# Optimization experiments

Hardware: AMD Instinct MI355X
Metric: run time of the kernel (lower is better)

Reference implementation:

```python
import jax, jax.numpy as jnp
import numpy as np
from jax import lax

E = 8          # num_experts
K = 2          # top-k
TASKS = 8
GATE_DIM = 16
# (in, expand, out, kernel, stride) per MoE stage
STAGES = [(3, 32, 16, 7, 2), (16, 64, 32, 3, 1), (32, 128, 64, 3, 2), (64, 256, 64, 3, 1), (64, 128, 32, 3, 1)]
DN = ('NCHW', 'OIHW', 'NCHW')


def _pw(x, w):
    return lax.conv_general_dilated(x, w, (1, 1), 'VALID', dimension_numbers=DN)


def _dw(x, w, s):
    p = w.shape[-1] // 2
    return lax.conv_general_dilated(x, w, (s, s), [(p, p), (p, p)], dimension_numbers=DN, feature_group_count=x.shape[1])


def _gn(x, scale, bias):
    # GroupNorm with num_groups = C // 4, eps = 1e-5 (torch default)
    B, C, H, W = x.shape
    G = C // 4
    xr = x.reshape(B, G, -1)
    m = xr.mean(-1, keepdims=True)
    v = xr.var(-1, keepdims=True)
    xn = ((xr - m) * lax.rsqrt(v + 1e-5)).reshape(B, C, H, W)
    return xn * scale[None, :, None, None] + bias[None, :, None, None]


def _dsc(x, p, stride):
    # DSCBlock: pw-conv -> GN -> SiLU -> dw-conv -> GN -> SiLU -> pw-conv -> GN
    w1, s1, b1, w2, s2, b2, w3, s3, b3 = p
    x = jax.nn.silu(_gn(_pw(x, w1), s1, b1))
    x = jax.nn.silu(_gn(_dw(x, w2, stride), s2, b2))
    return _gn(_pw(x, w3), s3, b3)


def _moe(gate_input, x, wg, p, stride, task_bh):
    # task-conditioned top-k softmax gating (noisy_gating=False, all aux loss weights 0)
    logits = gate_input @ wg[task_bh]                      # (B, E)
    probs = jax.nn.softmax(logits, axis=-1)
    topv, topi = lax.top_k(probs, K)
    topv = topv / topv.sum(-1, keepdims=True)              # renormalize top-k gates
    Bn = gate_input.shape[0]
    dense = jnp.zeros_like(probs).at[jnp.arange(Bn)[:, None], topi].set(topv)
    eo = jax.vmap(lambda pe: _dsc(x, pe, stride))(p)       # (E, B, C, H, W)
    return jnp.einsum('be,ebchw->bchw', dense, eo)


def _forward(fl, task_bh):
    gi, xi, ppe = fl[0], fl[1], fl[2]
    x = xi
    for i, (_, _, _, _, s) in enumerate(STAGES):
        base = 3 + i * 10
        wg = fl[base]
        p = tuple(fl[base + 1: base + 10])
        x = _moe(gi, x, wg, p, s, task_bh)
    Bn = x.shape[0]
    # patchify: (B,32,20,20) -> unfold(2,4,4).unfold(3,4,4) -> permute -> (B,25,512)
    patches = x.reshape(Bn, 32, 5, 4, 5, 4).transpose(0, 1, 2, 4, 3, 5)  # (B,32,5,5,4,4)
    patches = patches.transpose(0, 2, 3, 4, 5, 1).reshape(Bn, 25, 512)
    return patches + ppe


def setup_inputs():
    key = jax.random.key(0)
    ks = iter(jax.random.split(key, 256))
    B = 64
    d = {}
    d['gate_input'] = jax.random.normal(next(ks), (B, GATE_DIM), jnp.float32)
    d['expert_input'] = jax.random.normal(next(ks), (B, 3, 80, 80), jnp.float32)
    d['patch_pos_embed'] = 0.02 * jax.random.normal(next(ks), (1, 25, 512), jnp.float32)
    for i, (cin, exp, cout, k, s) in enumerate(STAGES, 1):
        d[f's{i}_wg'] = 0.1 * jax.random.normal(next(ks), (TASKS, GATE_DIM, E), jnp.float32)
        d[f's{i}_w1'] = jax.random.normal(next(ks), (E, exp, cin, 1, 1), jnp.float32) / np.sqrt(cin)
        d[f's{i}_g1s'] = 1.0 + 0.1 * jax.random.normal(next(ks), (E, exp), jnp.float32)
        d[f's{i}_g1b'] = 0.1 * jax.random.normal(next(ks), (E, exp), jnp.float32)
        d[f's{i}_w2'] = jax.random.normal(next(ks), (E, exp, 1, k, k), jnp.float32) / k
        d[f's{i}_g2s'] = 1.0 + 0.1 * jax.random.normal(next(ks), (E, exp), jnp.float32)
        d[f's{i}_g2b'] = 0.1 * jax.random.normal(next(ks), (E, exp), jnp.float32)
        d[f's{i}_w3'] = jax.random.normal(next(ks), (E, cout, exp, 1, 1), jnp.float32) / np.sqrt(exp)
        d[f's{i}_g3s'] = 1.0 + 0.1 * jax.random.normal(next(ks), (E, cout), jnp.float32)
        d[f's{i}_g3b'] = 0.1 * jax.random.normal(next(ks), (E, cout), jnp.float32)
    d['task_bh'] = 3
    return d


def reference(gate_input, expert_input, patch_pos_embed, s1_wg, s1_w1, s1_g1s, s1_g1b, s1_w2, s1_g2s, s1_g2b, s1_w3, s1_g3s, s1_g3b, s2_wg, s2_w1, s2_g1s, s2_g1b, s2_w2, s2_g2s, s2_g2b, s2_w3, s2_g3s, s2_g3b, s3_wg, s3_w1, s3_g1s, s3_g1b, s3_w2, s3_g2s, s3_g2b, s3_w3, s3_g3s, s3_g3b, s4_wg, s4_w1, s4_g1s, s4_g1b, s4_w2, s4_g2s, s4_g2b, s4_w3, s4_g3s, s4_g3b, s5_wg, s5_w1, s5_g1s, s5_g1b, s5_w2, s5_g2s, s5_g2b, s5_w3, s5_g3s, s5_g3b, task_bh):
    fl = (gate_input, expert_input, patch_pos_embed,
          s1_wg, s1_w1, s1_g1s, s1_g1b, s1_w2, s1_g2s, s1_g2b, s1_w3, s1_g3s, s1_g3b,
          s2_wg, s2_w1, s2_g1s, s2_g1b, s2_w2, s2_g2s, s2_g2b, s2_w3, s2_g3s, s2_g3b,
          s3_wg, s3_w1, s3_g1s, s3_g1b, s3_w2, s3_g2s, s3_g2b, s3_w3, s3_g3s, s3_g3b,
          s4_wg, s4_w1, s4_g1s, s4_g1b, s4_w2, s4_g2s, s4_g2b, s4_w3, s4_g3s, s4_g3b,
          s5_wg, s5_w1, s5_g1s, s5_g1b, s5_w2, s5_g2s, s5_g2b, s5_w3, s5_g3s, s5_g3b)
    patches = _forward(fl, task_bh)
    loss = jnp.zeros((), patches.dtype)  # all MoE loss weights are 0 in VisionEncoder
    return (patches, loss)
```

## Files before the change

### kernel.cpp

```cpp
#include <hip/hip_runtime.h>
#include <cstddef>

#define TPB 256

__device__ __forceinline__ int rfl(int v) { return __builtin_amdgcn_readfirstlane(v); }
__device__ __forceinline__ float rflf(float v) {
    return __int_as_float(__builtin_amdgcn_readfirstlane(__float_as_int(v)));
}

__device__ __forceinline__ unsigned short f2bf(float f) {
    union { float f; unsigned int u; } x{f};
    unsigned int r = x.u + 0x7fffu + ((x.u >> 16) & 1u);
    return (unsigned short)(r >> 16);
}
__device__ __forceinline__ float bf2f(unsigned short u) {
    return __uint_as_float(((unsigned int)u) << 16);
}

template <int N, int NW>
__device__ __forceinline__ void bredN(float* v, float* red) {
    __syncthreads();
    #pragma unroll
    for (int off = 32; off > 0; off >>= 1)
        #pragma unroll
        for (int i = 0; i < N; i++) v[i] += __shfl_down(v[i], off);
    const int lane = threadIdx.x & 63;
    const int wv = threadIdx.x >> 6;
    if (lane == 0)
        #pragma unroll
        for (int i = 0; i < N; i++) red[wv * N + i] = v[i];
    __syncthreads();
    if (threadIdx.x == 0) {
        #pragma unroll
        for (int i = 0; i < N; i++) {
            float s = 0.f;
            #pragma unroll
            for (int w = 0; w < NW; w++) s += red[w * N + i];
            red[i] = s;
        }
    }
    __syncthreads();
    #pragma unroll
    for (int i = 0; i < N; i++) v[i] = red[i];
}

__device__ __forceinline__ float silu_f(float v) {
    return v * __builtin_amdgcn_rcpf(1.f + __expf(-v));
}

struct GatePtrs { const float* wg[5]; };

__global__ void gate_kernel(const float* __restrict__ gi, GatePtrs gp,
                            const int* __restrict__ taskp,
                            int* __restrict__ gidx, float* __restrict__ gw) {
    const int s = blockIdx.x;
    const int b = threadIdx.x;
    const int task = taskp[0];
    const float* wg = gp.wg[s] + (size_t)task * 16 * 8;
    float l[8];
    #pragma unroll
    for (int e = 0; e < 8; e++) l[e] = 0.f;
    for (int d = 0; d < 16; d++) {
        float v = gi[b * 16 + d];
        #pragma unroll
        for (int e = 0; e < 8; e++) l[e] += v * wg[d * 8 + e];
    }
    float mx = l[0];
    #pragma unroll
    for (int e = 1; e < 8; e++) mx = fmaxf(mx, l[e]);
    float p[8]; float sum = 0.f;
    #pragma unroll
    for (int e = 0; e < 8; e++) { p[e] = expf(l[e] - mx); sum += p[e]; }
    int i0 = 0;
    #pragma unroll
    for (int e = 1; e < 8; e++) if (p[e] > p[i0]) i0 = e;
    int i1 = (i0 == 0) ? 1 : 0;
    #pragma unroll
    for (int e = 0; e < 8; e++) if (e != i0 && p[e] > p[i1]) i1 = e;
    const float denom = p[i0] + p[i1];
    const int base = (s * 64 + b) * 2;
    gidx[base] = i0; gidx[base + 1] = i1;
    gw[base] = p[i0] / denom; gw[base + 1] = p[i1] / denom;
}

template <int CIN, int CEXP, int KS, int STRIDE, int H, int W, int HO, int WO,
          int NCH, int TPBk>
__global__ __launch_bounds__(TPBk) void dsc_ab_v2(
    const float* __restrict__ xin, const float* __restrict__ w1,
    const float* __restrict__ g1s, const float* __restrict__ g1b,
    const float* __restrict__ w2,
    const float* __restrict__ g2s, const float* __restrict__ g2b,
    const int* __restrict__ gidx, unsigned short* __restrict__ act2) {
    constexpr int HW = H * W, HWO = HO * WO;
    constexpr int HP = H + 2, WPL = W + 3, EVW = (W + 2) / 2;
    constexpr int NPV = HW / 4;
    constexpr int JN = (NPV + TPBk - 1) / TPBk;
    constexpr int NW = TPBk / 64;
    constexpr int NG = NCH / 4;
    constexpr int Qc = HWO / 4;
    constexpr int QT = NCH * Qc;
    constexpr int QI = (QT + TPBk - 1) / TPBk;
    constexpr int KK = KS * KS;
    const int gch = blockIdx.x, b = blockIdx.y, slot = blockIdx.z;
    const int tid = threadIdx.x;
    const int e = rfl(gidx[b * 2 + slot]);
    const int cb0 = gch * NCH;

    __shared__ float buf1[NCH * HP * WPL];
    __shared__ float w2s[NCH * KK];
    __shared__ float sc2s[NCH], bi2s[NCH];
    __shared__ float red[2 * NG * NW];

    for (int i = tid; i < NCH * HP * WPL; i += TPBk) buf1[i] = 0.f;
    for (int i = tid; i < NCH * KK; i += TPBk) {
        int c = i / KK, k = i - c * KK;
        w2s[i] = w2[((size_t)e * CEXP + cb0 + c) * KK + k];
    }
    if (tid < NCH) {
        sc2s[tid] = g2s[e * CEXP + cb0 + tid];
        bi2s[tid] = g2b[e * CEXP + cb0 + tid];
    }

    const float* xb = xin + (size_t)b * CIN * HW;
    const float* w1e = w1 + ((size_t)e * CEXP + cb0) * CIN;

    float acc[NCH][JN][4];
    #pragma unroll
    for (int c = 0; c < NCH; c++)
        #pragma unroll
        for (int j = 0; j < JN; j++)
            #pragma unroll
            for (int t = 0; t < 4; t++) acc[c][j][t] = 0.f;

    for (int cb = 0; cb < CIN; cb += 4) {
        float wr[NCH][4];
        #pragma unroll
        for (int c = 0; c < NCH; c++)
            #pragma unroll
            for (int k = 0; k < 4; k++) wr[c][k] = rflf(w1e[c * CIN + cb + k]);
        #pragma unroll
        for (int j = 0; j < JN; j++) {
            const int pv = tid + j * TPBk;
            if (JN * TPBk == NPV || pv < NPV) {
                #pragma unroll
                for (int k = 0; k < 4; k++) {
                    const float4 v4 = *(const float4*)(xb + (cb + k) * HW + pv * 4);
                    const float va[4] = {v4.x, v4.y, v4.z, v4.w};
                    #pragma unroll
                    for (int c = 0; c < NCH; c++)
                        #pragma unroll
                        for (int t = 0; t < 4; t++)
                            acc[c][j][t] = fmaf(wr[c][k], va[t], acc[c][j][t]);
                }
            }
        }
    }
    float st[2 * NG];
    #pragma unroll
    for (int i = 0; i < 2 * NG; i++) st[i] = 0.f;
    #pragma unroll
    for (int c = 0; c < NCH; c++) {
        const int gs = (c >> 2) * 2;
        #pragma unroll
        for (int j = 0; j < JN; j++)
            #pragma unroll
            for (int t = 0; t < 4; t++) {
                float a = acc[c][j][t];
                st[gs] += a; st[gs + 1] += a * a;
            }
    }
    bredN<2 * NG, NW>(st, red);
    float mg[NG], ig[NG];
    #pragma unroll
    for (int g = 0; g < NG; g++) {
        mg[g] = st[g * 2] / (4.f * HW);
        float var = st[g * 2 + 1] / (4.f * HW) - mg[g] * mg[g];
        ig[g] = rsqrtf(var + 1e-5f);
    }
    float sc1r[NCH], bi1r[NCH];
    #pragma unroll
    for (int c = 0; c < NCH; c++) {
        sc1r[c] = rflf(g1s[e * CEXP + cb0 + c]);
        bi1r[c] = rflf(g1b[e * CEXP + cb0 + c]);
    }
    #pragma unroll
    for (int j = 0; j < JN; j++) {
        const int pv = tid + j * TPBk;
        if (JN * TPBk == NPV || pv < NPV) {
            const int p4 = pv * 4;
            const int ph = p4 / W, pwb = p4 - ph * W;
            #pragma unroll
            for (int c = 0; c < NCH; c++) {
                const int g = (NG == 1) ? 0 : (c >> 2);
                #pragma unroll
                for (int t = 0; t < 4; t++) {
                    float v = silu_f((acc[c][j][t] - mg[g]) * ig[g] * sc1r[c] + bi1r[c]);
                    const int j2 = pwb + t + 1;
                    const int col = (STRIDE == 1) ? j2
                                    : ((j2 & 1) ? EVW + (j2 >> 1) : (j2 >> 1));
                    buf1[(c * HP + ph + 1) * WPL + col] = v;
                }
            }
        }
    }
    __syncthreads();

    float dacc[QI][4];
    float st2[2 * NG];
    #pragma unroll
    for (int i = 0; i < 2 * NG; i++) st2[i] = 0.f;
    #pragma unroll
    for (int qi = 0; qi < QI; qi++) {
        #pragma unroll
        for (int t = 0; t < 4; t++) dacc[qi][t] = 0.f;
        const int q = tid + qi * TPBk;
        if (QI * TPBk == QT || q < QT) {
            const int c = q / Qc, qq = q - c * Qc;
            const int oh = qq % HO, owb = (qq / HO) * 4;
            float o[4] = {0.f, 0.f, 0.f, 0.f};
            if (STRIDE == 1) {
                #pragma unroll
                for (int kh = 0; kh < KS; kh++) {
                    const int base = (c * HP + oh + kh) * WPL + owb;
                    float r[6];
                    #pragma unroll
                    for (int i = 0; i < 6; i++) r[i] = buf1[base + i];
                    const float wa = w2s[c * KK + kh * KS + 0];
                    const float wb = w2s[c * KK + kh * KS + 1];
                    const float wcc = w2s[c * KK + kh * KS + 2];
                    #pragma unroll
                    for (int t = 0; t < 4; t++)
                        o[t] += wa * r[t] + wb * r[t + 1] + wcc * r[t + 2];
                }
            } else {
                #pragma unroll
                for (int kh = 0; kh < KS; kh++) {
                    const int base = (c * HP + 2 * oh + kh) * WPL;
                    float ev[5], od[4];
                    #pragma unroll
                    for (int i = 0; i < 5; i++) ev[i] = buf1[base + owb + i];
                    #pragma unroll
                    for (int i = 0; i < 4; i++) od[i] = buf1[base + EVW + owb + i];
                    const float wa = w2s[c * KK + kh * KS + 0];
                    const float wb = w2s[c * KK + kh * KS + 1];
                    const float wcc = w2s[c * KK + kh * KS + 2];
                    #pragma unroll
                    for (int t = 0; t < 4; t++)
                        o[t] += wa * ev[t] + wb * od[t] + wcc * ev[t + 1];
                }
            }
            #pragma unroll
            for (int t = 0; t < 4; t++) {
                float a = o[t];
                dacc[qi][t] = a;
                if constexpr (NG == 1) {
                    st2[0] += a; st2[1] += a * a;
                } else {
                    const bool gsel = (c >= 4);
                    float a0 = gsel ? 0.f : a, a1 = gsel ? a : 0.f;
                    st2[0] += a0; st2[1] += a0 * a0;
                    st2[2] += a1; st2[3] += a1 * a1;
                }
            }
        }
    }
    bredN<2 * NG, NW>(st2, red);
    float m2[NG], i2[NG];
    #pragma unroll
    for (int g = 0; g < NG; g++) {
        m2[g] = st2[g * 2] / (4.f * HWO);
        float var = st2[g * 2 + 1] / (4.f * HWO) - m2[g] * m2[g];
        i2[g] = rsqrtf(var + 1e-5f);
    }
    unsigned short* ao = act2 + ((size_t)(b * 2 + slot) * CEXP + cb0) * HWO;
    #pragma unroll
    for (int qi = 0; qi < QI; qi++) {
        const int q = tid + qi * TPBk;
        if (QI * TPBk == QT || q < QT) {
            const int c = q / Qc, qq = q - c * Qc;
            const int oh = qq % HO, owb = (qq / HO) * 4;
            const int g = (NG == 1) ? 0 : ((c >= 4) ? 1 : 0);
            const float sc = sc2s[c], bi = bi2s[c];
            ushort4 ov;
            ov.x = f2bf(silu_f((dacc[qi][0] - m2[g]) * i2[g] * sc + bi));
            ov.y = f2bf(silu_f((dacc[qi][1] - m2[g]) * i2[g] * sc + bi));
            ov.z = f2bf(silu_f((dacc[qi][2] - m2[g]) * i2[g] * sc + bi));
            ov.w = f2bf(silu_f((dacc[qi][3] - m2[g]) * i2[g] * sc + bi));
            *(ushort4*)(ao + c * HWO + oh * WO + owb) = ov;
        }
    }
}

__global__ __launch_bounds__(TPB) void dsc_ab_s1(
    const float* __restrict__ xin, const float* __restrict__ w1,
    const float* __restrict__ g1s, const float* __restrict__ g1b,
    const float* __restrict__ w2,
    const float* __restrict__ g2s, const float* __restrict__ g2b,
    const int* __restrict__ gidx, unsigned short* __restrict__ act2) {
    constexpr int H = 80, W = 80, HW = 6400, WO = 40, HWO = 1600;
    constexpr int CEXP = 32;
    constexpr int ROWS = 85, RW = 89, EV = 44;
    const int g = blockIdx.x, b = blockIdx.y, slot = blockIdx.z;
    const int tid = threadIdx.x;
    const int e = rfl(gidx[b * 2 + slot]);

    __shared__ float buf1[ROWS * RW];
    __shared__ float red[2 * (TPB / 64)];

    for (int i = tid; i < ROWS * RW; i += TPB) buf1[i] = 0.f;

    const float* xb = xin + (size_t)b * 3 * HW;
    const float* w1e = w1 + ((size_t)e * CEXP + g * 4) * 3;
    float wr[4][3];
    #pragma unroll
    for (int c = 0; c < 4; c++)
        #pragma unroll
        for (int k = 0; k < 3; k++) wr[c][k] = rflf(w1e[c * 3 + k]);

    float stv[2] = {0.f, 0.f};
    #pragma unroll
    for (int j = 0; j < 7; j++) {
        if (j < 6 || tid < 64) {
            int p4 = (j * TPB + tid) * 4;
            float4 v0 = *(const float4*)(xb + p4);
            float4 v1 = *(const float4*)(xb + HW + p4);
            float4 v2 = *(const float4*)(xb + 2 * HW + p4);
            float a0[4] = {v0.x, v0.y, v0.z, v0.w};
            float a1[4] = {v1.x, v1.y, v1.z, v1.w};
            float a2[4] = {v2.x, v2.y, v2.z, v2.w};
            #pragma unroll
            for (int t = 0; t < 4; t++) {
                #pragma unroll
                for (int c = 0; c < 4; c++) {
                    float a = fmaf(wr[c][0], a0[t], fmaf(wr[c][1], a1[t], wr[c][2] * a2[t]));
                    stv[0] += a; stv[1] += a * a;
                }
            }
        }
    }
    bredN<2, TPB / 64>(stv, red);
    const float mean = stv[0] / (4.f * HW);
    const float var = stv[1] / (4.f * HW) - mean * mean;
    const float inv = rsqrtf(var + 1e-5f);

    float dacc[4][2][4];
    float t1 = 0.f, t2 = 0.f;
    #pragma unroll
    for (int c = 0; c < 4; c++) {
        const float sc1 = rflf(g1s[e * CEXP + g * 4 + c]);
        const float bi1 = rflf(g1b[e * CEXP + g * 4 + c]);
        if (c > 0) __syncthreads();
        #pragma unroll
        for (int j = 0; j < 7; j++) {
            if (j < 6 || tid < 64) {
                int p4 = (j * TPB + tid) * 4;
                int ph = p4 / W, pwb = p4 - ph * W;
                float4 v0 = *(const float4*)(xb + p4);
                float4 v1 = *(const float4*)(xb + HW + p4);
                float4 v2 = *(const float4*)(xb + 2 * HW + p4);
                float a0[4] = {v0.x, v0.y, v0.z, v0.w};
                float a1[4] = {v1.x, v1.y, v1.z, v1.w};
                float a2[4] = {v2.x, v2.y, v2.z, v2.w};
                #pragma unroll
                for (int t = 0; t < 4; t++) {
                    float a = fmaf(wr[c][0], a0[t], fmaf(wr[c][1], a1[t], wr[c][2] * a2[t]));
                    float v = silu_f((a - mean) * inv * sc1 + bi1);
                    int j2 = pwb + t + 3;
                    buf1[(ph + 3) * RW + ((j2 & 1) ? EV + (j2 >> 1) : (j2 >> 1))] = v;
                }
            }
        }
        __syncthreads();
        const float* w2c = w2 + ((size_t)e * CEXP + g * 4 + c) * 49;
        float wc[49];
        #pragma unroll
        for (int k = 0; k < 49; k++) wc[k] = rflf(w2c[k]);
        #pragma unroll
        for (int qi = 0; qi < 2; qi++) {
            #pragma unroll
            for (int t = 0; t < 4; t++) dacc[c][qi][t] = 0.f;
            int q = tid + qi * TPB;
            if (q < 400) {
                int oh = q % 40, owb = (q / 40) * 4;
                float o[4] = {0.f, 0.f, 0.f, 0.f};
                #pragma unroll
                for (int kh = 0; kh < 7; kh++) {
                    const int base = (2 * oh + kh) * RW;
                    float evr[7], odr[6];
                    #pragma unroll
                    for (int i = 0; i < 7; i++) evr[i] = buf1[base + owb + i];
                    #pragma unroll
                    for (int i = 0; i < 6; i++) odr[i] = buf1[base + EV + owb + i];
                    #pragma unroll
                    for (int t = 0; t < 4; t++)
                        o[t] += wc[kh * 7 + 0] * evr[t]     + wc[kh * 7 + 1] * odr[t]
                              + wc[kh * 7 + 2] * evr[t + 1] + wc[kh * 7 + 3] * odr[t + 1]
                              + wc[kh * 7 + 4] * evr[t + 2] + wc[kh * 7 + 5] * odr[t + 2]
                              + wc[kh * 7 + 6] * evr[t + 3];
                }
                #pragma unroll
                for (int t = 0; t < 4; t++) {
                    dacc[c][qi][t] = o[t]; t1 += o[t]; t2 += o[t] * o[t];
                }
            }
        }
    }
    float st2v[2] = {t1, t2};
    bredN<2, TPB / 64>(st2v, red);
    const float mean2 = st2v[0] / (4.f * HWO);
    const float var2 = st2v[1] / (4.f * HWO) - mean2 * mean2;
    const float inv2 = rsqrtf(var2 + 1e-5f);
    unsigned short* ao = act2 + ((size_t)(b * 2 + slot) * CEXP + g * 4) * HWO;
    #pragma unroll
    for (int c = 0; c < 4; c++) {
        const float sc2 = rflf(g2s[e * CEXP + g * 4 + c]);
        const float bi2 = rflf(g2b[e * CEXP + g * 4 + c]);
        #pragma unroll
        for (int qi = 0; qi < 2; qi++) {
            int q = tid + qi * TPB;
            if (q < 400) {
                int oh = q % 40, owb = (q / 40) * 4;
                ushort4 ov;
                ov.x = f2bf(silu_f((dacc[c][qi][0] - mean2) * inv2 * sc2 + bi2));
                ov.y = f2bf(silu_f((dacc[c][qi][1] - mean2) * inv2 * sc2 + bi2));
                ov.z = f2bf(silu_f((dacc[c][qi][2] - mean2) * inv2 * sc2 + bi2));
                ov.w = f2bf(silu_f((dacc[c][qi][3] - mean2) * inv2 * sc2 + bi2));
                *(ushort4*)(ao + c * HWO + oh * WO + owb) = ov;
            }
        }
    }
}


template <int CEXP, int COUT, int HWO, int MT, int NT, int VEC, int PXC>
__global__ __launch_bounds__(256) void pw3_k1(
    const unsigned short* __restrict__ act2, const float* __restrict__ w3,
    const int* __restrict__ gidx,
    float* __restrict__ raw3, float* __restrict__ statsw) {
    constexpr int NTILE = NT * VEC;
    static_assert(MT * NT == 256 && NTILE == 64, "tile");
    constexpr int G = COUT / 4;
    constexpr int KC = 16;
    constexpr int WPT = (KC * COUT) / 256;
    const int pxc = blockIdx.x, b = blockIdx.y, slot = blockIdx.z;
    const int tid = threadIdx.x;
    const int e = rfl(gidx[b * 2 + slot]);
    const int px0 = pxc * NTILE;
    const int ct = tid / NT, pt = tid % NT;

    __shared__ float actT[KC][NTILE];
    __shared__ float wT[KC][COUT];

    const unsigned short* ab = act2 + (size_t)(b * 2 + slot) * CEXP * HWO;
    const float* w3e = w3 + (size_t)e * COUT * CEXP;

    float acc[4][VEC];
    #pragma unroll
    for (int i = 0; i < 4; i++)
        #pragma unroll
        for (int j = 0; j < VEC; j++) acc[i][j] = 0.f;

    const int lkk = tid / 16;
    const int lp4 = (tid % 16) * 4;
    const int wc = tid / (KC / WPT);
    const int wk = (tid % (KC / WPT)) * WPT;

    for (int k0 = 0; k0 < CEXP; k0 += KC) {
        __syncthreads();
        {
            const int px = px0 + lp4;
            ushort4 v = make_ushort4(0, 0, 0, 0);
            if (px < HWO) v = *(const ushort4*)(ab + (size_t)(k0 + lkk) * HWO + px);
            float4 f = {bf2f(v.x), bf2f(v.y), bf2f(v.z), bf2f(v.w)};
            *(float4*)&actT[lkk][lp4] = f;
        }
        #pragma unroll
        for (int i = 0; i < WPT; i++)
            wT[wk + i][wc] = w3e[(size_t)wc * CEXP + k0 + wk + i];
        __syncthreads();
        #pragma unroll
        for (int kk = 0; kk < KC; kk++) {
            const float4 w4 = *(const float4*)&wT[kk][ct * 4];
            const float wf[4] = {w4.x, w4.y, w4.z, w4.w};
            float av[VEC];
            if constexpr (VEC == 4) {
                float4 a4 = *(const float4*)&actT[kk][pt * 4];
                av[0] = a4.x; av[1] = a4.y; av[2] = a4.z; av[3] = a4.w;
            } else if constexpr (VEC == 2) {
                float2 a2 = *(const float2*)&actT[kk][pt * 2];
                av[0] = a2.x; av[1] = a2.y;
            } else {
                av[0] = actT[kk][pt];
            }
            #pragma unroll
            for (int i = 0; i < 4; i++)
                #pragma unroll
                for (int j = 0; j < VEC; j++)
                    acc[i][j] = fmaf(wf[i], av[j], acc[i][j]);
        }
    }

    const int px = px0 + pt * VEC;
    float s1 = 0.f, s2 = 0.f;
    #pragma unroll
    for (int i = 0; i < 4; i++) {
        if (px < HWO) {
            float* rp = raw3 + ((size_t)(b * 2 + slot) * COUT + ct * 4 + i) * HWO + px;
            if constexpr (VEC == 4) {
                float4 v = {acc[i][0], acc[i][1], acc[i][2], acc[i][3]};
                *(float4*)rp = v;
            } else if constexpr (VEC == 2) {
                float2 v = {acc[i][0], acc[i][1]};
                *(float2*)rp = v;
            } else {
                *rp = acc[i][0];
            }
        }
        #pragma unroll
        for (int j = 0; j < VEC; j++) { s1 += acc[i][j]; s2 += acc[i][j] * acc[i][j]; }
    }
    #pragma unroll
    for (int off = NT / 2; off > 0; off >>= 1) {
        s1 += __shfl_down(s1, off);
        s2 += __shfl_down(s2, off);
    }
    if (pt == 0) {
        float* sp = statsw + (((size_t)(b * 2 + slot) * G + ct) * PXC + pxc) * 2;
        sp[0] = s1; sp[1] = s2;
    }
}

template <int COUT, int HWO, int PXC>
__global__ void pw3_k2(const float* __restrict__ statsw,
                       const float* __restrict__ g3s, const float* __restrict__ g3b,
                       const int* __restrict__ gidx, const float* __restrict__ gw,
                       float* __restrict__ ABw) {
    constexpr int G = COUT / 4;
    const int b = blockIdx.x;
    const int t = threadIdx.x;
    const int slot = t / COUT, c = t - slot * COUT, g = c >> 2;
    const int e = gidx[b * 2 + slot];
    const float wgt = gw[b * 2 + slot];
    const float* sp = statsw + ((size_t)(b * 2 + slot) * G + g) * PXC * 2;
    float s1 = 0.f, s2 = 0.f;
    for (int i = 0; i < PXC; i++) { s1 += sp[i * 2]; s2 += sp[i * 2 + 1]; }
    const float mean = s1 / (4.f * HWO);
    const float var = s2 / (4.f * HWO) - mean * mean;
    const float inv = rsqrtf(var + 1e-5f);
    const float sc = g3s[e * COUT + c], bi = g3b[e * COUT + c];
    float* abp = ABw + ((size_t)(b * 2 + slot) * COUT + c) * 2;
    abp[0] = wgt * inv * sc;
    abp[1] = wgt * (bi - mean * inv * sc);
}

template <int COUT, int HWO>
__global__ __launch_bounds__(256) void pw3_k3(const float* __restrict__ raw3,
                                              const float* __restrict__ ABw,
                                              float* __restrict__ xout) {
    constexpr int PH4 = HWO / 4;
    constexpr int N4 = 64 * COUT * PH4;
    const int idx = blockIdx.x * 256 + threadIdx.x;
    if (idx >= N4) return;
    const int b = idx / (COUT * PH4);
    const int r = idx - b * COUT * PH4;
    const int c = r / PH4, p4 = (r - c * PH4) * 4;
    const float* r0 = raw3 + ((size_t)(b * 2 + 0) * COUT + c) * HWO + p4;
    const float* r1 = raw3 + ((size_t)(b * 2 + 1) * COUT + c) * HWO + p4;
    const float* ab0 = ABw + ((size_t)(b * 2 + 0) * COUT + c) * 2;
    const float* ab1 = ABw + ((size_t)(b * 2 + 1) * COUT + c) * 2;
    const float A0 = ab0[0], B0 = ab0[1], A1 = ab1[0], B1 = ab1[1];
    const float4 v0 = *(const float4*)r0, v1 = *(const float4*)r1;
    float4 o;
    o.x = fmaf(A0, v0.x, B0) + fmaf(A1, v1.x, B1);
    o.y = fmaf(A0, v0.y, B0) + fmaf(A1, v1.y, B1);
    o.z = fmaf(A0, v0.z, B0) + fmaf(A1, v1.z, B1);
    o.w = fmaf(A0, v0.w, B0) + fmaf(A1, v1.w, B1);
    *(float4*)(xout + ((size_t)b * COUT + c) * HWO + p4) = o;
}

__global__ void patchify_kernel(const float* __restrict__ x, const float* __restrict__ ppe,
                                float* __restrict__ out) {
    const int idx = blockIdx.x * TPB + threadIdx.x;
    if (idx < 64 * 25 * 512) {
        int d = idx & 511;
        int p = (idx >> 9) % 25;
        int b = idx / (25 * 512);
        int c = d & 31;
        int j = (d >> 5) & 3;
        int i = d >> 7;
        int ph = p / 5, pw = p % 5;
        out[idx] = x[((b * 32 + c) * 20 + ph * 4 + i) * 20 + pw * 4 + j] + ppe[p * 512 + d];
    }
    if (idx == 0) out[64 * 25 * 512] = 0.f;
}

extern "C" void kernel_launch(void* const* d_in, const int* in_sizes, int n_in,
                              void* d_out, int out_size, void* d_ws, size_t ws_size,
                              hipStream_t stream) {
    const float* gate_input = (const float*)d_in[0];
    const float* expert_input = (const float*)d_in[1];
    const float* ppe = (const float*)d_in[2];
    const int* taskp = (const int*)d_in[53];
    auto in = [&](int s, int k) { return (const float*)d_in[3 + s * 10 + k]; };

    char* ws = (char*)d_ws;
    int* gidx = (int*)ws;
    float* gw = (float*)(ws + 4096);
    float* x0 = (float*)(ws + 8192);
    float* x1 = (float*)(ws + 8192 + 6553600);
    unsigned short* act2 = (unsigned short*)(ws + 8192 + 6553600 + 13107200);
    float* raw3 = (float*)(ws + 8192 + 6553600 + 13107200 + 26214400);
    float* statsw = (float*)(ws + 8192 + 6553600 + 13107200 + 2 * 26214400);
    float* ABw = (float*)(ws + 8192 + 6553600 + 13107200 + 2 * 26214400 + 1048576);

    GatePtrs gp;
    for (int s = 0; s < 5; s++) gp.wg[s] = in(s, 0);
    gate_kernel<<<5, 64, 0, stream>>>(gate_input, gp, taskp, gidx, gw);

    dsc_ab_s1<<<dim3(8, 64, 2), TPB, 0, stream>>>(
        expert_input, in(0, 1), in(0, 2), in(0, 3), in(0, 4), in(0, 5), in(0, 6),
        gidx + 0 * 128, act2);
    pw3_k1<32, 16, 1600, 4, 64, 1, 25><<<dim3(25, 64, 2), 256, 0, stream>>>(
        act2, in(0, 7), gidx + 0 * 128, raw3, statsw);
    pw3_k2<16, 1600, 25><<<64, 32, 0, stream>>>(
        statsw, in(0, 8), in(0, 9), gidx + 0 * 128, gw + 0 * 128, ABw);
    pw3_k3<16, 1600><<<(64 * 16 * 400 + 255) / 256, 256, 0, stream>>>(raw3, ABw, x0);

    dsc_ab_v2<16, 64, 3, 1, 40, 40, 40, 40, 4, 256><<<dim3(16, 64, 2), 256, 0, stream>>>(
        x0, in(1, 1), in(1, 2), in(1, 3), in(1, 4), in(1, 5), in(1, 6),
        gidx + 1 * 128, act2);
    pw3_k1<64, 32, 1600, 8, 32, 2, 25><<<dim3(25, 64, 2), 256, 0, stream>>>(
        act2, in(1, 7), gidx + 1 * 128, raw3, statsw);
    pw3_k2<32, 1600, 25><<<64, 64, 0, stream>>>(
        statsw, in(1, 8), in(1, 9), gidx + 1 * 128, gw + 1 * 128, ABw);
    pw3_k3<32, 1600><<<(64 * 32 * 400 + 255) / 256, 256, 0, stream>>>(raw3, ABw, x1);

    dsc_ab_v2<32, 128, 3, 2, 40, 40, 20, 20, 4, 256><<<dim3(32, 64, 2), 256, 0, stream>>>(
        x1, in(2, 1), in(2, 2), in(2, 3), in(2, 4), in(2, 5), in(2, 6),
        gidx + 2 * 128, act2);
    pw3_k1<128, 64, 400, 16, 16, 4, 7><<<dim3(7, 64, 2), 256, 0, stream>>>(
        act2, in(2, 7), gidx + 2 * 128, raw3, statsw);
    pw3_k2<64, 400, 7><<<64, 128, 0, stream>>>(
        statsw, in(2, 8), in(2, 9), gidx + 2 * 128, gw + 2 * 128, ABw);
    pw3_k3<64, 400><<<(64 * 64 * 100 + 255) / 256, 256, 0, stream>>>(raw3, ABw, x0);

    dsc_ab_v2<64, 256, 3, 1, 20, 20, 20, 20, 8, 128><<<dim3(32, 64, 2), 128, 0, stream>>>(
        x0, in(3, 1), in(3, 2), in(3, 3), in(3, 4), in(3, 5), in(3, 6),
        gidx + 3 * 128, act2);
    pw3_k1<256, 64, 400, 16, 16, 4, 7><<<dim3(7, 64, 2), 256, 0, stream>>>(
        act2, in(3, 7), gidx + 3 * 128, raw3, statsw);
    pw3_k2<64, 400, 7><<<64, 128, 0, stream>>>(
        statsw, in(3, 8), in(3, 9), gidx + 3 * 128, gw + 3 * 128, ABw);
    pw3_k3<64, 400><<<(64 * 64 * 100 + 255) / 256, 256, 0, stream>>>(raw3, ABw, x1);

    dsc_ab_v2<64, 128, 3, 1, 20, 20, 20, 20, 8, 128><<<dim3(16, 64, 2), 128, 0, stream>>>(
        x1, in(4, 1), in(4, 2), in(4, 3), in(4, 4), in(4, 5), in(4, 6),
        gidx + 4 * 128, act2);
    pw3_k1<128, 32, 400, 8, 32, 2, 7><<<dim3(7, 64, 2), 256, 0, stream>>>(
        act2, in(4, 7), gidx + 4 * 128, raw3, statsw);
    pw3_k2<32, 400, 7><<<64, 64, 0, stream>>>(
        statsw, in(4, 8), in(4, 9), gidx + 4 * 128, gw + 4 * 128, ABw);
    pw3_k3<32, 400><<<(64 * 32 * 100 + 255) / 256, 256, 0, stream>>>(raw3, ABw, x0);

    patchify_kernel<<<(64 * 25 * 512 + TPB - 1) / TPB, TPB, 0, stream>>>(x0, ppe, (float*)d_out);
}
```

Measured before the change: 551.6 us.

## Store stage-1 expanded activations as bf16 in LDS and fuse GN3/combine/patchify kernels

In the stage-1 kernel, the expanded pointwise output for all four channels is now computed once, stored as bf16 in shared memory, and normalized in place. Before, the input was reloaded and recomputed for each channel, with a barrier between channels. The separate GN3 stats kernel, affine-combine kernel and final patchify kernel are merged into one kernel per stage, and the last stage writes straight into the patch layout with the positional embedding added. This cuts global reloads, barriers and kernel launches. In exchange, the pre-norm activations are rounded to bf16 and shared memory use grows.

```diff
diff --git a/kernel.cpp b/kernel.cpp
--- a/kernel.cpp
+++ b/kernel.cpp
@@ -299,15 +299,18 @@
     const int* __restrict__ gidx, unsigned short* __restrict__ act2) {
     constexpr int H = 80, W = 80, HW = 6400, WO = 40, HWO = 1600;
     constexpr int CEXP = 32;
-    constexpr int ROWS = 85, RW = 89, EV = 44;
+    constexpr int ROWS = 85, EV = 43, RW = 89;
     const int g = blockIdx.x, b = blockIdx.y, slot = blockIdx.z;
     const int tid = threadIdx.x;
     const int e = rfl(gidx[b * 2 + slot]);
 
-    __shared__ float buf1[ROWS * RW];
+    __shared__ unsigned short sb[4 * ROWS * RW];
     __shared__ float red[2 * (TPB / 64)];
 
-    for (int i = tid; i < ROWS * RW; i += TPB) buf1[i] = 0.f;
+    {
+        unsigned int* sb32 = (unsigned int*)sb;
+        for (int i = tid; i < (4 * ROWS * RW) / 2; i += TPB) sb32[i] = 0u;
+    }
 
     const float* xb = xin + (size_t)b * 3 * HW;
     const float* w1e = w1 + ((size_t)e * CEXP + g * 4) * 3;
@@ -321,20 +324,29 @@
     #pragma unroll
     for (int j = 0; j < 7; j++) {
         if (j < 6 || tid < 64) {
-            int p4 = (j * TPB + tid) * 4;
-            float4 v0 = *(const float4*)(xb + p4);
-            float4 v1 = *(const float4*)(xb + HW + p4);
-            float4 v2 = *(const float4*)(xb + 2 * HW + p4);
-            float a0[4] = {v0.x, v0.y, v0.z, v0.w};
-            float a1[4] = {v1.x, v1.y, v1.z, v1.w};
-            float a2[4] = {v2.x, v2.y, v2.z, v2.w};
-            #pragma unroll
-            for (int t = 0; t < 4; t++) {
-                #pragma unroll
-                for (int c = 0; c < 4; c++) {
-                    float a = fmaf(wr[c][0], a0[t], fmaf(wr[c][1], a1[t], wr[c][2] * a2[t]));
-                    stv[0] += a; stv[1] += a * a;
-                }
+            const int p4 = (j * TPB + tid) * 4;
+            const float4 v0 = *(const float4*)(xb + p4);
+            const float4 v1 = *(const float4*)(xb + HW + p4);
+            const float4 v2 = *(const float4*)(xb + 2 * HW + p4);
+            const float a0[4] = {v0.x, v0.y, v0.z, v0.w};
+            const float a1[4] = {v1.x, v1.y, v1.z, v1.w};
+            const float a2[4] = {v2.x, v2.y, v2.z, v2.w};
+            const int ph = p4 / W, pwb = p4 - ph * W;
+            const int ebase = (ph + 3) * RW + (pwb >> 1) + 2;
+            const int obase = (ph + 3) * RW + EV + (pwb >> 1) + 1;
+            #pragma unroll
+            for (int c = 0; c < 4; c++) {
+                float at[4];
+                #pragma unroll
+                for (int t = 0; t < 4; t++) {
+                    at[t] = fmaf(wr[c][0], a0[t], fmaf(wr[c][1], a1[t], wr[c][2] * a2[t]));
+                    stv[0] += at[t]; stv[1] += at[t] * at[t];
+                }
+                const int cb = c * (ROWS * RW);
+                sb[cb + obase]     = f2bf(at[0]);
+                sb[cb + ebase]     = f2bf(at[1]);
+                sb[cb + obase + 1] = f2bf(at[2]);
+                sb[cb + ebase + 1] = f2bf(at[3]);
             }
         }
     }
@@ -342,35 +354,38 @@
     const float mean = stv[0] / (4.f * HW);
     const float var = stv[1] / (4.f * HW) - mean * mean;
     const float inv = rsqrtf(var + 1e-5f);
+    float sc1r[4], bi1r[4];
+    #pragma unroll
+    for (int c = 0; c < 4; c++) {
+        sc1r[c] = rflf(g1s[e * CEXP + g * 4 + c]);
+        bi1r[c] = rflf(g1b[e * CEXP + g * 4 + c]);
+    }
+
+    #pragma unroll
+    for (int j = 0; j < 7; j++) {
+        if (j < 6 || tid < 64) {
+            const int p4 = (j * TPB + tid) * 4;
+            const int ph = p4 / W, pwb = p4 - ph * W;
+            const int ebase = (ph + 3) * RW + (pwb >> 1) + 2;
+            const int obase = (ph + 3) * RW + EV + (pwb >> 1) + 1;
+            #pragma unroll
+            for (int c = 0; c < 4; c++) {
+                const int cb = c * (ROWS * RW);
+                const int idx4[4] = {cb + obase, cb + ebase, cb + obase + 1, cb + ebase + 1};
+                #pragma unroll
+                for (int t = 0; t < 4; t++) {
+                    float x = bf2f(sb[idx4[t]]);
+                    sb[idx4[t]] = f2bf(silu_f((x - mean) * inv * sc1r[c] + bi1r[c]));
+                }
+            }
+        }
+    }
+    __syncthreads();
 
     float dacc[4][2][4];
     float t1 = 0.f, t2 = 0.f;
     #pragma unroll
     for (int c = 0; c < 4; c++) {
-        const float sc1 = rflf(g1s[e * CEXP + g * 4 + c]);
-        const float bi1 = rflf(g1b[e * CEXP + g * 4 + c]);
-        if (c > 0) __syncthreads();
-        #pragma unroll
-        for (int j = 0; j < 7; j++) {
-            if (j < 6 || tid < 64) {
-                int p4 = (j * TPB + tid) * 4;
-                int ph = p4 / W, pwb = p4 - ph * W;
-                float4 v0 = *(const float4*)(xb + p4);
-                float4 v1 = *(const float4*)(xb + HW + p4);
-                float4 v2 = *(const float4*)(xb + 2 * HW + p4);
-                float a0[4] = {v0.x, v0.y, v0.z, v0.w};
-                float a1[4] = {v1.x, v1.y, v1.z, v1.w};
-                float a2[4] = {v2.x, v2.y, v2.z, v2.w};
-                #pragma unroll
-                for (int t = 0; t < 4; t++) {
-                    float a = fmaf(wr[c][0], a0[t], fmaf(wr[c][1], a1[t], wr[c][2] * a2[t]));
-                    float v = silu_f((a - mean) * inv * sc1 + bi1);
-                    int j2 = pwb + t + 3;
-                    buf1[(ph + 3) * RW + ((j2 & 1) ? EV + (j2 >> 1) : (j2 >> 1))] = v;
-                }
-            }
-        }
-        __syncthreads();
         const float* w2c = w2 + ((size_t)e * CEXP + g * 4 + c) * 49;
         float wc[49];
         #pragma unroll
@@ -379,18 +394,18 @@
         for (int qi = 0; qi < 2; qi++) {
             #pragma unroll
             for (int t = 0; t < 4; t++) dacc[c][qi][t] = 0.f;
-            int q = tid + qi * TPB;
+            const int q = tid + qi * TPB;
             if (q < 400) {
-                int oh = q % 40, owb = (q / 40) * 4;
+                const int oh = q % 40, owb = (q / 40) * 4;
                 float o[4] = {0.f, 0.f, 0.f, 0.f};
                 #pragma unroll
                 for (int kh = 0; kh < 7; kh++) {
-                    const int base = (2 * oh + kh) * RW;
+                    const int base = c * (ROWS * RW) + (2 * oh + kh) * RW;
                     float evr[7], odr[6];
                     #pragma unroll
-                    for (int i = 0; i < 7; i++) evr[i] = buf1[base + owb + i];
-                    #pragma unroll
-                    for (int i = 0; i < 6; i++) odr[i] = buf1[base + EV + owb + i];
+                    for (int i = 0; i < 7; i++) evr[i] = bf2f(sb[base + owb + i]);
+                    #pragma unroll
+                    for (int i = 0; i < 6; i++) odr[i] = bf2f(sb[base + EV + owb + i]);
                     #pragma unroll
                     for (int t = 0; t < 4; t++)
                         o[t] += wc[kh * 7 + 0] * evr[t]     + wc[kh * 7 + 1] * odr[t]
@@ -417,9 +432,9 @@
         const float bi2 = rflf(g2b[e * CEXP + g * 4 + c]);
         #pragma unroll
         for (int qi = 0; qi < 2; qi++) {
-            int q = tid + qi * TPB;
+            const int q = tid + qi * TPB;
             if (q < 400) {
-                int oh = q % 40, owb = (q / 40) * 4;
+                const int oh = q % 40, owb = (q / 40) * 4;
                 ushort4 ov;
                 ov.x = f2bf(silu_f((dacc[c][qi][0] - mean2) * inv2 * sc2 + bi2));
                 ov.y = f2bf(silu_f((dacc[c][qi][1] - mean2) * inv2 * sc2 + bi2));
@@ -530,68 +545,68 @@
     }
 }
 
-template <int COUT, int HWO, int PXC>
-__global__ void pw3_k2(const float* __restrict__ statsw,
-                       const float* __restrict__ g3s, const float* __restrict__ g3b,
-                       const int* __restrict__ gidx, const float* __restrict__ gw,
-                       float* __restrict__ ABw) {
+template <int COUT, int HWO, int PXC, bool PATCH>
+__global__ __launch_bounds__(256) void pw3_k3m(
+    const float* __restrict__ raw3, const float* __restrict__ statsw,
+    const float* __restrict__ g3s, const float* __restrict__ g3b,
+    const int* __restrict__ gidx, const float* __restrict__ gw,
+    const float* __restrict__ ppe, float* __restrict__ out) {
     constexpr int G = COUT / 4;
-    const int b = blockIdx.x;
-    const int t = threadIdx.x;
-    const int slot = t / COUT, c = t - slot * COUT, g = c >> 2;
-    const int e = gidx[b * 2 + slot];
-    const float wgt = gw[b * 2 + slot];
-    const float* sp = statsw + ((size_t)(b * 2 + slot) * G + g) * PXC * 2;
-    float s1 = 0.f, s2 = 0.f;
-    for (int i = 0; i < PXC; i++) { s1 += sp[i * 2]; s2 += sp[i * 2 + 1]; }
-    const float mean = s1 / (4.f * HWO);
-    const float var = s2 / (4.f * HWO) - mean * mean;
-    const float inv = rsqrtf(var + 1e-5f);
-    const float sc = g3s[e * COUT + c], bi = g3b[e * COUT + c];
-    float* abp = ABw + ((size_t)(b * 2 + slot) * COUT + c) * 2;
-    abp[0] = wgt * inv * sc;
-    abp[1] = wgt * (bi - mean * inv * sc);
-}
-
-template <int COUT, int HWO>
-__global__ __launch_bounds__(256) void pw3_k3(const float* __restrict__ raw3,
-                                              const float* __restrict__ ABw,
-                                              float* __restrict__ xout) {
-    constexpr int PH4 = HWO / 4;
-    constexpr int N4 = 64 * COUT * PH4;
-    const int idx = blockIdx.x * 256 + threadIdx.x;
-    if (idx >= N4) return;
-    const int b = idx / (COUT * PH4);
-    const int r = idx - b * COUT * PH4;
-    const int c = r / PH4, p4 = (r - c * PH4) * 4;
-    const float* r0 = raw3 + ((size_t)(b * 2 + 0) * COUT + c) * HWO + p4;
-    const float* r1 = raw3 + ((size_t)(b * 2 + 1) * COUT + c) * HWO + p4;
-    const float* ab0 = ABw + ((size_t)(b * 2 + 0) * COUT + c) * 2;
-    const float* ab1 = ABw + ((size_t)(b * 2 + 1) * COUT + c) * 2;
-    const float A0 = ab0[0], B0 = ab0[1], A1 = ab1[0], B1 = ab1[1];
-    const float4 v0 = *(const float4*)r0, v1 = *(const float4*)r1;
-    float4 o;
-    o.x = fmaf(A0, v0.x, B0) + fmaf(A1, v1.x, B1);
-    o.y = fmaf(A0, v0.y, B0) + fmaf(A1, v1.y, B1);
-    o.z = fmaf(A0, v0.z, B0) + fmaf(A1, v1.z, B1);
-    o.w = fmaf(A0, v0.w, B0) + fmaf(A1, v1.w, B1);
-    *(float4*)(xout + ((size_t)b * COUT + c) * HWO + p4) = o;
-}
-
-__global__ void patchify_kernel(const float* __restrict__ x, const float* __restrict__ ppe,
-                                float* __restrict__ out) {
-    const int idx = blockIdx.x * TPB + threadIdx.x;
-    if (idx < 64 * 25 * 512) {
-        int d = idx & 511;
-        int p = (idx >> 9) % 25;
-        int b = idx / (25 * 512);
-        int c = d & 31;
-        int j = (d >> 5) & 3;
-        int i = d >> 7;
-        int ph = p / 5, pw = p % 5;
-        out[idx] = x[((b * 32 + c) * 20 + ph * 4 + i) * 20 + pw * 4 + j] + ppe[p * 512 + d];
-    }
-    if (idx == 0) out[64 * 25 * 512] = 0.f;
+    constexpr int Q = HWO / 4;
+    const int gg = blockIdx.x, b = blockIdx.y;
+    const int tid = threadIdx.x;
+
+    float A[2][4], Bv[2][4];
+    #pragma unroll
+    for (int slot = 0; slot < 2; slot++) {
+        const int e = rfl(gidx[b * 2 + slot]);
+        const float wgt = rflf(gw[b * 2 + slot]);
+        const float* sp = statsw + ((size_t)(b * 2 + slot) * G + gg) * PXC * 2;
+        float s1 = 0.f, s2 = 0.f;
+        for (int i = 0; i < PXC; i++) { s1 += sp[i * 2]; s2 += sp[i * 2 + 1]; }
+        const float mean = s1 / (4.f * HWO);
+        const float var = s2 / (4.f * HWO) - mean * mean;
+        const float inv = rsqrtf(var + 1e-5f);
+        #pragma unroll
+        for (int i = 0; i < 4; i++) {
+            const int c = gg * 4 + i;
+            const float sc = rflf(g3s[e * COUT + c]);
+            const float bi = rflf(g3b[e * COUT + c]);
+            A[slot][i] = wgt * inv * sc;
+            Bv[slot][i] = wgt * (bi - mean * inv * sc);
+        }
+    }
+
+    #pragma unroll
+    for (int i = 0; i < 4; i++) {
+        const int c = gg * 4 + i;
+        const float* r0 = raw3 + ((size_t)(b * 2 + 0) * COUT + c) * HWO;
+        const float* r1 = raw3 + ((size_t)(b * 2 + 1) * COUT + c) * HWO;
+        for (int q = tid; q < Q; q += 256) {
+            const int p4 = q * 4;
+            const float4 v0 = *(const float4*)(r0 + p4);
+            const float4 v1 = *(const float4*)(r1 + p4);
+            float o[4];
+            o[0] = fmaf(A[0][i], v0.x, Bv[0][i]) + fmaf(A[1][i], v1.x, Bv[1][i]);
+            o[1] = fmaf(A[0][i], v0.y, Bv[0][i]) + fmaf(A[1][i], v1.y, Bv[1][i]);
+            o[2] = fmaf(A[0][i], v0.z, Bv[0][i]) + fmaf(A[1][i], v1.z, Bv[1][i]);
+            o[3] = fmaf(A[0][i], v0.w, Bv[0][i]) + fmaf(A[1][i], v1.w, Bv[1][i]);
+            if constexpr (!PATCH) {
+                float4 ov = {o[0], o[1], o[2], o[3]};
+                *(float4*)(out + ((size_t)b * COUT + c) * HWO + p4) = ov;
+            } else {
+                const int ph = p4 / 20, pw0 = p4 - ph * 20;
+                const int p = (ph >> 2) * 5 + (pw0 >> 2);
+                const int dbase = ((ph & 3) * 4) * 32 + c;
+                float* op = out + ((size_t)b * 25 + p) * 512;
+                const float* pp = ppe + p * 512;
+                #pragma unroll
+                for (int jj = 0; jj < 4; jj++)
+                    op[dbase + jj * 32] = o[jj] + pp[dbase + jj * 32];
+            }
+        }
+    }
+    if (PATCH && gg == 0 && b == 0 && tid == 0) out[64 * 25 * 512] = 0.f;
 }
 
 extern "C" void kernel_launch(void* const* d_in, const int* in_sizes, int n_in,
@@ -611,7 +626,7 @@
     unsigned short* act2 = (unsigned short*)(ws + 8192 + 6553600 + 13107200);
     float* raw3 = (float*)(ws + 8192 + 6553600 + 13107200 + 26214400);
     float* statsw = (float*)(ws + 8192 + 6553600 + 13107200 + 2 * 26214400);
-    float* ABw = (float*)(ws + 8192 + 6553600 + 13107200 + 2 * 26214400 + 1048576);
+    float* outp = (float*)d_out;
 
     GatePtrs gp;
     for (int s = 0; s < 5; s++) gp.wg[s] = in(s, 0);
@@ -622,45 +637,38 @@
         gidx + 0 * 128, act2);
     pw3_k1<32, 16, 1600, 4, 64, 1, 25><<<dim3(25, 64, 2), 256, 0, stream>>>(
         act2, in(0, 7), gidx + 0 * 128, raw3, statsw);
-    pw3_k2<16, 1600, 25><<<64, 32, 0, stream>>>(
-        statsw, in(0, 8), in(0, 9), gidx + 0 * 128, gw + 0 * 128, ABw);
-    pw3_k3<16, 1600><<<(64 * 16 * 400 + 255) / 256, 256, 0, stream>>>(raw3, ABw, x0);
+    pw3_k3m<16, 1600, 25, false><<<dim3(4, 64), 256, 0, stream>>>(
+        raw3, statsw, in(0, 8), in(0, 9), gidx + 0 * 128, gw + 0 * 128, ppe, x0);
 
     dsc_ab_v2<16, 64, 3, 1, 40, 40, 40, 40, 4, 256><<<dim3(16, 64, 2), 256, 0, stream>>>(
         x0, in(1, 1), in(1, 2), in(1, 3), in(1, 4), in(1, 5), in(1, 6),
         gidx + 1 * 128, act2);
     pw3_k1<64, 32, 1600, 8, 32, 2, 25><<<dim3(25, 64, 2), 256, 0, stream>>>(
         act2, in(1, 7), gidx + 1 * 128, raw3, statsw);
-    pw3_k2<32, 1600, 25><<<64, 64, 0, stream>>>(
-        statsw, in(1, 8), in(1, 9), gidx + 1 * 128, gw + 1 * 128, ABw);
-    pw3_k3<32, 1600><<<(64 * 32 * 400 + 255) / 256, 256, 0, stream>>>(raw3, ABw, x1);
+    pw3_k3m<32, 1600, 25, false><<<dim3(8, 64), 256, 0, stream>>>(
+        raw3, statsw, in(1, 8), in(1, 9), gidx + 1 * 128, gw + 1 * 128, ppe, x1);
 
     dsc_ab_v2<32, 128, 3, 2, 40, 40, 20, 20, 4, 256><<<dim3(32, 64, 2), 256, 0, stream>>>(
         x1, in(2, 1), in(2, 2), in(2, 3), in(2, 4), in(2, 5), in(2, 6),
         gidx + 2 * 128, act2);
     pw3_k1<128, 64, 400, 16, 16, 4, 7><<<dim3(7, 64, 2), 256, 0, stream>>>(
         act2, in(2, 7), gidx + 2 * 128, raw3, statsw);
-    pw3_k2<64, 400, 7><<<64, 128, 0, stream>>>(
-        statsw, in(2, 8), in(2, 9), gidx + 2 * 128, gw + 2 * 128, ABw);
-    pw3_k3<64, 400><<<(64 * 64 * 100 + 255) / 256, 256, 0, stream>>>(raw3, ABw, x0);
+    pw3_k3m<64, 400, 7, false><<<dim3(16, 64), 256, 0, stream>>>(
+        raw3, statsw, in(2, 8), in(2, 9), gidx + 2 * 128, gw + 2 * 128, ppe, x0);
 
     dsc_ab_v2<64, 256, 3, 1, 20, 20, 20, 20, 8, 128><<<dim3(32, 64, 2), 128, 0, stream>>>(
         x0, in(3, 1), in(3, 2), in(3, 3), in(3, 4), in(3, 5), in(3, 6),
         gidx + 3 * 128, act2);
     pw3_k1<256, 64, 400, 16, 16, 4, 7><<<dim3(7, 64, 2), 256, 0, stream>>>(
         act2, in(3, 7), gidx + 3 * 128, raw3, statsw);
-    pw3_k2<64, 400, 7><<<64, 128, 0, stream>>>(
-        statsw, in(3, 8), in(3, 9), gidx + 3 * 128, gw + 3 * 128, ABw);
-    pw3_k3<64, 400><<<(64 * 64 * 100 + 255) / 256, 256, 0, stream>>>(raw3, ABw, x1);
+    pw3_k3m<64, 400, 7, false><<<dim3(16, 64), 256, 0, stream>>>(
+        raw3, statsw, in(3, 8), in(3, 9), gidx + 3 * 128, gw + 3 * 128, ppe, x1);
 
     dsc_ab_v2<64, 128, 3, 1, 20, 20, 20, 20, 8, 128><<<dim3(16, 64, 2), 128, 0, stream>>>(
         x1, in(4, 1), in(4, 2), in(4, 3), in(4, 4), in(4, 5), in(4, 6),
         gidx + 4 * 128, act2);
     pw3_k1<128, 32, 400, 8, 32, 2, 7><<<dim3(7, 64, 2), 256, 0, stream>>>(
         act2, in(4, 7), gidx + 4 * 128, raw3, statsw);
-    pw3_k2<32, 400, 7><<<64, 64, 0, stream>>>(
-        statsw, in(4, 8), in(4, 9), gidx + 4 * 128, gw + 4 * 128, ABw);
-    pw3_k3<32, 400><<<(64 * 32 * 100 + 255) / 256, 256, 0, stream>>>(raw3, ABw, x0);
-
-    patchify_kernel<<<(64 * 25 * 512 + TPB - 1) / TPB, TPB, 0, stream>>>(x0, ppe, (float*)d_out);
-}
+    pw3_k3m<32, 400, 7, true><<<dim3(8, 64), 256, 0, stream>>>(
+        raw3, statsw, in(4, 8), in(4, 9), gidx + 4 * 128, gw + 4 * 128, ppe, outp);
+}
```

New measurement: 686.9 us. 24.5% more time.
